# Kernel optimization log

Hardware: AMD Instinct MI355X
Metric: run time of the kernel (lower is better)

## Reference

```python
import jax, jax.numpy as jnp
import numpy as np

BS, SEQ, D_MODEL = 4, 1024, 4096
N_Q_HEADS, N_KV_HEADS, D_K, D_V = 32, 8, 128, 128
ROPE_BASE = 10000.0


def _rotate_half(x):
    x1, x2 = jnp.split(x, 2, axis=-1)
    return jnp.concatenate([-x2, x1], axis=-1)


def _apply_rope(x, pos0):
    # x: [bs, heads, seq, d]; positions pos0 .. pos0+seq-1
    d = x.shape[-1]
    seq = x.shape[2]
    inv_freq = 1.0 / (ROPE_BASE ** (jnp.arange(0, d, 2, dtype=jnp.float32) / d))  # [d/2]
    pos = (pos0 + jnp.arange(seq)).astype(jnp.float32)  # [seq]
    ang = pos[:, None] * inv_freq[None, :]  # [seq, d/2]
    cos = jnp.concatenate([jnp.cos(ang), jnp.cos(ang)], axis=-1)  # [seq, d]
    sin = jnp.concatenate([jnp.sin(ang), jnp.sin(ang)], axis=-1)
    return x * cos[None, None] + _rotate_half(x) * sin[None, None]


def setup_inputs() -> dict:
    key = jax.random.key(0)
    ks = jax.random.split(key, 8)
    w_scale = 0.02  # keep logits in a sane range (original uses raw normal init)
    return {
        "query": jax.random.normal(ks[0], (BS, SEQ, D_MODEL), dtype=jnp.float32),
        "key": jax.random.normal(ks[1], (BS, SEQ, D_MODEL), dtype=jnp.float32),
        "value": jax.random.normal(ks[2], (BS, SEQ, D_MODEL), dtype=jnp.float32),
        "mask": jnp.zeros((BS, SEQ, SEQ), dtype=jnp.float32),
        "wq": jax.random.normal(ks[3], (D_MODEL, N_Q_HEADS * D_K), dtype=jnp.float32) * w_scale,
        "wk": jax.random.normal(ks[4], (D_MODEL, N_KV_HEADS * D_K), dtype=jnp.float32) * w_scale,
        "wv": jax.random.normal(ks[5], (D_MODEL, N_KV_HEADS * D_V), dtype=jnp.float32) * w_scale,
        "wo": jax.random.normal(ks[6], (N_Q_HEADS * D_V, D_MODEL), dtype=jnp.float32) * w_scale,
        "curr_seq_pos": 0,
    }


def reference(query, key, value, mask, wq, wk, wv, wo, curr_seq_pos):
    bs, sq, _ = query.shape
    n_groups = N_Q_HEADS // N_KV_HEADS
    # projections -> [bs, heads, seq, d]
    q = (query @ wq).reshape(bs, sq, N_Q_HEADS, D_K).transpose((0, 2, 1, 3))
    sk = key.shape[1]
    k = (key @ wk).reshape(bs, sk, N_KV_HEADS, 1, D_K)
    k = jnp.repeat(k, n_groups, axis=3).reshape(bs, sk, N_Q_HEADS, D_K).transpose((0, 2, 1, 3))
    v = (value @ wv).reshape(bs, sk, N_KV_HEADS, 1, D_V)
    v = jnp.repeat(v, n_groups, axis=3).reshape(bs, sk, N_Q_HEADS, D_V).transpose((0, 2, 1, 3))
    scale = jnp.sqrt(jnp.float32(D_K))
    q = _apply_rope(q, curr_seq_pos)
    k = _apply_rope(k, curr_seq_pos)
    # [bs, h, sq, sk]
    raw = jnp.einsum("bhqd,bhkd->bhqk", q, k) / scale
    masked = raw + mask[:bs, None, curr_seq_pos:curr_seq_pos + sq, :sk]
    attn = jax.nn.softmax(masked, axis=-1)
    out = jnp.einsum("bhqk,bhkd->bhqd", attn, v)
    out = out.transpose((0, 2, 1, 3)).reshape(bs, sq, N_Q_HEADS * D_V)
    return out @ wo
```

## Files before the change

### kernel.cpp

```cpp
#include <hip/hip_runtime.h>


using ushort = unsigned short;
typedef __attribute__((ext_vector_type(8))) short short8;
typedef __attribute__((ext_vector_type(4))) short short4v;
typedef __attribute__((ext_vector_type(4))) float f32x4;

__device__ __forceinline__ ushort f2bf(float x) {
  unsigned int u = __float_as_uint(x);
  u += 0x7FFFu + ((u >> 16) & 1u);
  return (ushort)(u >> 16);
}
__device__ __forceinline__ float bf2f(ushort h) {
  return __uint_as_float(((unsigned int)h) << 16);
}

__device__ __forceinline__ void async_copy16(const void* g, void* l) {
  __builtin_amdgcn_global_load_lds((const __attribute__((address_space(1))) void*)g,
                                   (__attribute__((address_space(3))) void*)l, 16, 0, 0);
}

__global__ __launch_bounds__(256)
void cvt_f32_bf16(const float* __restrict__ in, ushort* __restrict__ out, int n4) {
  const int i = blockIdx.x * 256 + threadIdx.x;
  if (i < n4) {
    const float4 f = ((const float4*)in)[i];
    short4v v;
    v[0] = (short)f2bf(f.x); v[1] = (short)f2bf(f.y);
    v[2] = (short)f2bf(f.z); v[3] = (short)f2bf(f.w);
    ((short4v*)out)[i] = v;
  }
}

__global__ __launch_bounds__(256)
void transpose_cvt(const float* __restrict__ B, ushort* __restrict__ Bt, int N) {
  __shared__ ushort t[64][72];
  const int n0 = blockIdx.x * 64, k0 = blockIdx.y * 64;
  const int tid = threadIdx.x;
  const int r = tid >> 3, c8 = (tid & 7) * 8;
#pragma unroll
  for (int p = 0; p < 2; p++) {
    const float* src = B + (size_t)(k0 + r + p * 32) * N + n0 + c8;
    const float4 f0 = *(const float4*)src;
    const float4 f1 = *(const float4*)(src + 4);
    ushort* d = &t[r + p * 32][c8];
    d[0] = f2bf(f0.x); d[1] = f2bf(f0.y); d[2] = f2bf(f0.z); d[3] = f2bf(f0.w);
    d[4] = f2bf(f1.x); d[5] = f2bf(f1.y); d[6] = f2bf(f1.z); d[7] = f2bf(f1.w);
  }
  __syncthreads();
#pragma unroll
  for (int p = 0; p < 2; p++) {
    const int n = r + p * 32;
    short8 o;
#pragma unroll
    for (int j = 0; j < 8; j++) o[j] = (short)t[c8 + j][n];
    *(short8*)(Bt + (size_t)(n0 + n) * 4096 + k0 + c8) = o;
  }
}

template <int MODE, bool AF32>
__global__ __launch_bounds__(256, 2)
void gemm_bt(const float* __restrict__ Af, const float* __restrict__ A2f,
             const ushort* __restrict__ Abf, const ushort* __restrict__ Bt,
             ushort* __restrict__ C, ushort* __restrict__ C2,
             float* __restrict__ Cf, const int* __restrict__ posp,
             int N, float scale) {
  constexpr int K = 4096;
  __shared__ alignas(16) ushort As[128 * 32];
  __shared__ alignas(16) ushort Bs[128 * 32];
  const int tid = threadIdx.x;
  const int wave = tid >> 6, lane = tid & 63;
  const int quad = lane >> 4, l16 = lane & 15;
  const int m0 = blockIdx.y * 128, n0 = blockIdx.x * 128;
  const int wm = (wave & 1) * 64, wn2 = (wave >> 1) * 32;

  const size_t aoff = (size_t)(m0 + wave * 16 + (lane >> 2)) * K + (lane & 3) * 8;
  const float* gAf = nullptr;
  const ushort* gAb = nullptr;
  if constexpr (AF32) {
    const float* Ause = Af;
    if constexpr (MODE == 4) {
      if (n0 >= 1024) Ause = A2f;
    }
    gAf = Ause + aoff;
  } else {
    gAb = Abf + aoff;
  }
  const ushort* gB = Bt + (size_t)(n0 + wave * 16 + (lane >> 2)) * K + (lane & 3) * 8;
  ushort* lA = As + wave * 512;
  ushort* lB = Bs + wave * 512;
  constexpr size_t rstep = (size_t)64 * K;

  f32x4 acc[4][4] = {};

  for (int kt = 0; kt < K; kt += 32) {
    if constexpr (AF32) {
      const float4 a0 = *(const float4*)(gAf + kt);
      const float4 a1 = *(const float4*)(gAf + kt + 4);
      const float4 b0 = *(const float4*)(gAf + rstep + kt);
      const float4 b1 = *(const float4*)(gAf + rstep + kt + 4);
      short8 v0, v1;
      v0[0] = (short)f2bf(a0.x); v0[1] = (short)f2bf(a0.y);
      v0[2] = (short)f2bf(a0.z); v0[3] = (short)f2bf(a0.w);
      v0[4] = (short)f2bf(a1.x); v0[5] = (short)f2bf(a1.y);
      v0[6] = (short)f2bf(a1.z); v0[7] = (short)f2bf(a1.w);
      v1[0] = (short)f2bf(b0.x); v1[1] = (short)f2bf(b0.y);
      v1[2] = (short)f2bf(b0.z); v1[3] = (short)f2bf(b0.w);
      v1[4] = (short)f2bf(b1.x); v1[5] = (short)f2bf(b1.y);
      v1[6] = (short)f2bf(b1.z); v1[7] = (short)f2bf(b1.w);
      *(short8*)(lA + lane * 8) = v0;
      *(short8*)(lA + 2048 + lane * 8) = v1;
    } else {
      async_copy16(gAb + kt, lA);
      async_copy16(gAb + rstep + kt, lA + 2048);
    }
    async_copy16(gB + kt, lB);
    async_copy16(gB + rstep + kt, lB + 2048);
    __syncthreads();
    short8 af[4], bfrag[4];
#pragma unroll
    for (int i = 0; i < 4; i++) {
      af[i] = *(const short8*)(As + (wm + i * 16 + l16) * 32 + quad * 8);
      bfrag[i] = *(const short8*)(
          Bs + (wn2 + (i & 1) * 16 + (i >> 1) * 64 + l16) * 32 + quad * 8);
    }
#pragma unroll
    for (int i = 0; i < 4; i++)
#pragma unroll
      for (int j = 0; j < 4; j++)
        acc[i][j] = __builtin_amdgcn_mfma_f32_16x16x32_bf16(af[i], bfrag[j],
                                                            acc[i][j], 0, 0, 0);
    __syncthreads();
  }

  if constexpr (MODE == 0) {
#pragma unroll
    for (int i = 0; i < 4; i++)
#pragma unroll
      for (int j = 0; j < 4; j++) {
        const int n = n0 + wn2 + (j & 1) * 16 + (j >> 1) * 64 + l16;
        const int mb = m0 + wm + i * 16 + quad * 4;
#pragma unroll
        for (int r = 0; r < 4; r++)
          Cf[(size_t)(mb + r) * N + n] = acc[i][j][r] * scale;
      }
  } else {
    const bool kv_v = (MODE == 4) && (n0 >= 1024);
    if (!kv_v) {
      const int pos0 = posp[0];
      const int h = (MODE == 1) ? (n0 >> 7) : (n0 >> 7);
      const int NH = (MODE == 1) ? 32 : 8;
      constexpr float lgbase = -0.20762050593045983f;
      float invf[2];
      invf[0] = exp2f((float)(wn2 + l16) * lgbase);
      invf[1] = exp2f((float)(wn2 + 16 + l16) * lgbase);
#pragma unroll
      for (int i = 0; i < 4; i++) {
#pragma unroll
        for (int r = 0; r < 4; r++) {
          const int m = m0 + wm + i * 16 + quad * 4 + r;
          const int s = m & 1023, bb = m >> 10;
          const float p = (float)(s + pos0);
          ushort* row = C + (((size_t)bb * NH + h) * 1024 + s) * 128;
#pragma unroll
          for (int jj = 0; jj < 2; jj++) {
            float sn, cs;
            sincosf(p * invf[jj], &sn, &cs);
            const float x1 = acc[i][jj][r] * scale;
            const float x2 = acc[i][jj + 2][r] * scale;
            const int dlo = wn2 + jj * 16 + l16;
            row[dlo] = f2bf(x1 * cs - x2 * sn);
            row[dlo + 64] = f2bf(x2 * cs + x1 * sn);
          }
        }
      }
    } else {
      const int hh = (n0 - 1024) >> 7;
#pragma unroll
      for (int i = 0; i < 4; i++)
#pragma unroll
        for (int j = 0; j < 4; j++) {
          const int d = wn2 + (j & 1) * 16 + (j >> 1) * 64 + l16;
          const int mb = m0 + wm + i * 16 + quad * 4;
#pragma unroll
          for (int r = 0; r < 4; r++) {
            const int m = mb + r;
            const int bb = m >> 10, s = m & 1023;
            C2[(((size_t)bb * 8 + hh) * 128 + d) * 1024 + s] = f2bf(acc[i][j][r]);
          }
        }
    }
  }
}

__global__ __launch_bounds__(256, 2)
void attn_kernel(const ushort* __restrict__ Qh, const ushort* __restrict__ Kh,
                 const ushort* __restrict__ Vt, const ushort* __restrict__ Mk,
                 ushort* __restrict__ Oh) {
  __shared__ alignas(16) ushort Qs[64 * 128];
  __shared__ alignas(16) ushort Ks[64 * 128];
  __shared__ alignas(16) ushort Vs[128 * 64];
  __shared__ alignas(16) ushort Ms[64 * 64];
  ushort* Ps = Ks;
  const int b = blockIdx.z, h = blockIdx.y;
  const int q0 = blockIdx.x * 64;
  const int hkv = h >> 2;
  const int tid = threadIdx.x;
  const int wave = tid >> 6, lane = tid & 63;
  const int quad = lane >> 4, l16 = lane & 15;

  const ushort* Qg = Qh + (((size_t)b * 32 + h) * 1024 + q0) * 128;
  const ushort* Kg = Kh + ((size_t)b * 8 + hkv) * (size_t)(1024 * 128);
  const ushort* Vg = Vt + ((size_t)b * 8 + hkv) * (size_t)(128 * 1024);
  const ushort* Mg = Mk + ((size_t)b * 1024 + q0) * 1024;

#pragma unroll
  for (int c = 0; c < 4; c++) {
    const int i = wave * 4 + c;
    const int row = i * 4 + (lane >> 4);
    const int kc = (lane & 15) ^ (c * 4 + (lane >> 4));
    async_copy16(Qg + (size_t)row * 128 + kc * 8, Qs + i * 512);
  }

  float m_i[4], l_i[4];
#pragma unroll
  for (int r = 0; r < 4; r++) { m_i[r] = -1e30f; l_i[r] = 0.0f; }
  f32x4 acc_o[8] = {};

  const int vr = lane >> 3;
  const int vkc = (lane & 7) ^ (vr & 7);

  for (int kt = 0; kt < 1024; kt += 64) {
#pragma unroll
    for (int c = 0; c < 4; c++) {
      const int i = wave * 4 + c;
      const int row = i * 4 + (lane >> 4);
      const int kc = (lane & 15) ^ (c * 4 + (lane >> 4));
      async_copy16(Kg + (size_t)(kt + row) * 128 + kc * 8, Ks + i * 512);
    }
#pragma unroll
    for (int c = 0; c < 4; c++) {
      const int i = wave * 4 + c;
      async_copy16(Vg + (size_t)(i * 8 + vr) * 1024 + kt + vkc * 8, Vs + i * 512);
    }
#pragma unroll
    for (int c = 0; c < 2; c++)
      async_copy16(Mg + (size_t)(wave * 8 + c * 32 + vr) * 1024 + kt + (lane & 7) * 8,
                   Ms + wave * 512 + c * 2048);
    __syncthreads();

    f32x4 s[4] = {};
    const int qrow = (wave * 16 + l16) * 128;
#pragma unroll
    for (int ks = 0; ks < 4; ks++) {
      const int ko = ((ks * 4 + quad) ^ l16) * 8;
      const short8 aq = *(const short8*)(Qs + qrow + ko);
#pragma unroll
      for (int nt = 0; nt < 4; nt++) {
        const short8 bk = *(const short8*)(Ks + (nt * 16 + l16) * 128 + ko);
        s[nt] = __builtin_amdgcn_mfma_f32_16x16x32_bf16(aq, bk, s[nt], 0, 0, 0);
      }
    }
    __syncthreads();

#pragma unroll
    for (int nt = 0; nt < 4; nt++)
#pragma unroll
      for (int r = 0; r < 4; r++)
        s[nt][r] += bf2f(Ms[(wave * 16 + quad * 4 + r) * 64 + nt * 16 + l16]);

    float al[4];
#pragma unroll
    for (int r = 0; r < 4; r++) {
      float mx = fmaxf(fmaxf(s[0][r], s[1][r]), fmaxf(s[2][r], s[3][r]));
#pragma unroll
      for (int off = 1; off < 16; off <<= 1) mx = fmaxf(mx, __shfl_xor(mx, off));
      const float mnew = fmaxf(m_i[r], mx);
      al[r] = __expf(m_i[r] - mnew);
      float sum = 0.0f;
#pragma unroll
      for (int nt = 0; nt < 4; nt++) {
        const float pv = __expf(s[nt][r] - mnew);
        s[nt][r] = pv;
        sum += pv;
      }
#pragma unroll
      for (int off = 1; off < 16; off <<= 1) sum += __shfl_xor(sum, off);
      l_i[r] = l_i[r] * al[r] + sum;
      m_i[r] = mnew;
    }
#pragma unroll
    for (int dt = 0; dt < 8; dt++)
#pragma unroll
      for (int r = 0; r < 4; r++) acc_o[dt][r] *= al[r];

#pragma unroll
    for (int nt = 0; nt < 4; nt++)
#pragma unroll
      for (int r = 0; r < 4; r++)
        Ps[wave * 1152 + (quad * 4 + r) * 72 + nt * 16 + l16] = f2bf(s[nt][r]);
    __asm__ volatile("s_waitcnt lgkmcnt(0)" ::: "memory");

#pragma unroll
    for (int kk = 0; kk < 2; kk++) {
      const short8 ap = *(const short8*)(Ps + wave * 1152 + l16 * 72 + kk * 32 + quad * 8);
#pragma unroll
      for (int dt = 0; dt < 8; dt++) {
        const int vo = ((kk * 4 + quad) ^ (l16 & 7)) * 8;
        const short8 bv = *(const short8*)(Vs + (dt * 16 + l16) * 64 + vo);
        acc_o[dt] = __builtin_amdgcn_mfma_f32_16x16x32_bf16(ap, bv, acc_o[dt], 0, 0, 0);
      }
    }
    __syncthreads();
  }

  ushort* Og = Oh + ((size_t)b * 1024 + q0 + wave * 16) * 4096 + h * 128;
#pragma unroll
  for (int r = 0; r < 4; r++) {
    const float inv = 1.0f / l_i[r];
#pragma unroll
    for (int dt = 0; dt < 8; dt++)
      Og[(size_t)(quad * 4 + r) * 4096 + dt * 16 + l16] = f2bf(acc_o[dt][r] * inv);
  }
}

extern "C" void kernel_launch(void* const* d_in, const int* in_sizes, int n_in,
                              void* d_out, int out_size, void* d_ws, size_t ws_size,
                              hipStream_t stream) {
  (void)in_sizes; (void)n_in; (void)out_size; (void)ws_size;
  const float* query = (const float*)d_in[0];
  const float* key = (const float*)d_in[1];
  const float* value = (const float*)d_in[2];
  const float* mask = (const float*)d_in[3];
  const float* wq = (const float*)d_in[4];
  const float* wk = (const float*)d_in[5];
  const float* wv = (const float*)d_in[6];
  const float* wo = (const float*)d_in[7];
  const int* pos = (const int*)d_in[8];
  float* out = (float*)d_out;

  char* ws = (char*)d_ws;
  const size_t MB = 1024 * 1024;
  ushort* qb = (ushort*)(ws + 0 * MB);
  ushort* Khb = (ushort*)(ws + 0 * MB);
  ushort* Vtb = (ushort*)(ws + 8 * MB);
  ushort* wqT = (ushort*)(ws + 32 * MB);
  ushort* wkvT = (ushort*)(ws + 32 * MB);
  ushort* Ohb = (ushort*)(ws + 32 * MB);
  ushort* Qhb = (ushort*)(ws + 64 * MB);
  ushort* woT = (ushort*)(ws + 64 * MB);
  ushort* mbf = (ushort*)(ws + 96 * MB);

  dim3 blk(256);
  cvt_f32_bf16<<<dim3(4096), blk, 0, stream>>>(mask, mbf, 1048576);
  cvt_f32_bf16<<<dim3(16384), blk, 0, stream>>>(query, qb, 4194304);

  transpose_cvt<<<dim3(64, 64), blk, 0, stream>>>(wq, wqT, 4096);
  gemm_bt<1, false><<<dim3(32, 32), blk, 0, stream>>>(
      nullptr, nullptr, qb, wqT, Qhb, nullptr, nullptr, pos, 4096,
      0.08838834764831845f);

  transpose_cvt<<<dim3(16, 64), blk, 0, stream>>>(wk, wkvT, 1024);
  transpose_cvt<<<dim3(16, 64), blk, 0, stream>>>(wv, wkvT + (size_t)1024 * 4096, 1024);
  gemm_bt<4, true><<<dim3(16, 32), blk, 0, stream>>>(
      key, value, nullptr, wkvT, Khb, Vtb, nullptr, pos, 2048, 1.0f);

  attn_kernel<<<dim3(16, 32, 4), blk, 0, stream>>>(Qhb, Khb, Vtb, mbf, Ohb);

  transpose_cvt<<<dim3(64, 64), blk, 0, stream>>>(wo, woT, 4096);
  gemm_bt<0, false><<<dim3(32, 32), blk, 0, stream>>>(
      nullptr, nullptr, Ohb, woT, nullptr, nullptr, out, pos, 4096, 1.0f);
}
```

Measured before the change: 964.8 us.

## Restructure attention kernel with 128-row tiles, double-buffered K/V and lazy rescale

The attention kernel now processes 128 query rows per block (32 per wave) with Q held in registers. It double-buffers K/V tiles in LDS so the next tile loads while the current one computes, and reads the mask directly from global memory into registers. It skips the online-softmax rescale unless the row max grows by more than a threshold, defers the row-sum reduction to the end, and swizzles the P buffer. These changes cut per-iteration syncs and load latency and raise MFMA reuse of K/V, at the cost of more registers and possibly lower occupancy.

```diff
diff --git a/kernel.cpp b/kernel.cpp
--- a/kernel.cpp
+++ b/kernel.cpp
@@ -197,17 +197,22 @@
 void attn_kernel(const ushort* __restrict__ Qh, const ushort* __restrict__ Kh,
                  const ushort* __restrict__ Vt, const ushort* __restrict__ Mk,
                  ushort* __restrict__ Oh) {
-  __shared__ alignas(16) ushort Qs[64 * 128];
-  __shared__ alignas(16) ushort Ks[64 * 128];
-  __shared__ alignas(16) ushort Vs[128 * 64];
-  __shared__ alignas(16) ushort Ms[64 * 64];
-  ushort* Ps = Ks;
+  __shared__ alignas(16) ushort smem[40960];
+  ushort* const Ks0 = smem;
+  ushort* const Ks1 = smem + 8192;
+  ushort* const Vs0 = smem + 16384;
+  ushort* const Vs1 = smem + 24576;
+  ushort* const Ps = smem + 32768;
+  ushort* const Qtmp = smem + 16384;
+
   const int b = blockIdx.z, h = blockIdx.y;
-  const int q0 = blockIdx.x * 64;
+  const int q0 = blockIdx.x * 128;
   const int hkv = h >> 2;
   const int tid = threadIdx.x;
   const int wave = tid >> 6, lane = tid & 63;
   const int quad = lane >> 4, l16 = lane & 15;
+  const int vr = lane >> 3;
+  const int vkc = (lane & 7) ^ (vr & 7);
 
   const ushort* Qg = Qh + (((size_t)b * 32 + h) * 1024 + q0) * 128;
   const ushort* Kg = Kh + ((size_t)b * 8 + hkv) * (size_t)(1024 * 128);
@@ -215,113 +220,174 @@
   const ushort* Mg = Mk + ((size_t)b * 1024 + q0) * 1024;
 
 #pragma unroll
+  for (int c = 0; c < 8; c++) {
+    const int i = wave * 8 + c;
+    const int row = i * 4 + quad;
+    const int kc = l16 ^ ((c & 3) * 4 + quad);
+    async_copy16(Qg + (size_t)row * 128 + kc * 8, Qtmp + i * 512);
+  }
+#pragma unroll
   for (int c = 0; c < 4; c++) {
     const int i = wave * 4 + c;
-    const int row = i * 4 + (lane >> 4);
-    const int kc = (lane & 15) ^ (c * 4 + (lane >> 4));
-    async_copy16(Qg + (size_t)row * 128 + kc * 8, Qs + i * 512);
-  }
-
-  float m_i[4], l_i[4];
-#pragma unroll
-  for (int r = 0; r < 4; r++) { m_i[r] = -1e30f; l_i[r] = 0.0f; }
-  f32x4 acc_o[8] = {};
-
-  const int vr = lane >> 3;
-  const int vkc = (lane & 7) ^ (vr & 7);
+    const int row = i * 4 + quad;
+    const int kc = l16 ^ (c * 4 + quad);
+    async_copy16(Kg + (size_t)row * 128 + kc * 8, Ks0 + i * 512);
+  }
+  __asm__ volatile("s_waitcnt vmcnt(0)" ::: "memory");
+  short8 qreg[2][4];
+#pragma unroll
+  for (int t = 0; t < 2; t++)
+#pragma unroll
+    for (int ks = 0; ks < 4; ks++)
+      qreg[t][ks] = *(const short8*)(Qtmp + (size_t)(wave * 32 + t * 16 + l16) * 128 +
+                                     (((ks * 4 + quad) ^ l16) * 8));
+  __syncthreads();
+#pragma unroll
+  for (int c = 0; c < 4; c++) {
+    const int i = wave * 4 + c;
+    async_copy16(Vg + (size_t)(i * 8 + vr) * 1024 + vkc * 8, Vs0 + i * 512);
+  }
+
+  float m_i[2][4], l_p[2][4];
+#pragma unroll
+  for (int t = 0; t < 2; t++)
+#pragma unroll
+    for (int r = 0; r < 4; r++) { m_i[t][r] = -1e30f; l_p[t][r] = 0.0f; }
+  f32x4 acc[2][8] = {};
+
+  ushort* const PW = Ps + wave * 2048;
 
   for (int kt = 0; kt < 1024; kt += 64) {
-#pragma unroll
-    for (int c = 0; c < 4; c++) {
-      const int i = wave * 4 + c;
-      const int row = i * 4 + (lane >> 4);
-      const int kc = (lane & 15) ^ (c * 4 + (lane >> 4));
-      async_copy16(Kg + (size_t)(kt + row) * 128 + kc * 8, Ks + i * 512);
-    }
-#pragma unroll
-    for (int c = 0; c < 4; c++) {
-      const int i = wave * 4 + c;
-      async_copy16(Vg + (size_t)(i * 8 + vr) * 1024 + kt + vkc * 8, Vs + i * 512);
-    }
-#pragma unroll
-    for (int c = 0; c < 2; c++)
-      async_copy16(Mg + (size_t)(wave * 8 + c * 32 + vr) * 1024 + kt + (lane & 7) * 8,
-                   Ms + wave * 512 + c * 2048);
+    const int it = kt >> 6;
+    ushort* const Kc = (it & 1) ? Ks1 : Ks0;
+    ushort* const Vc = (it & 1) ? Vs1 : Vs0;
+    ushort* const Kn = (it & 1) ? Ks0 : Ks1;
+    ushort* const Vn = (it & 1) ? Vs0 : Vs1;
     __syncthreads();
 
-    f32x4 s[4] = {};
-    const int qrow = (wave * 16 + l16) * 128;
+    ushort mr[2][4][4];
+#pragma unroll
+    for (int t = 0; t < 2; t++)
+#pragma unroll
+      for (int nt = 0; nt < 4; nt++)
+#pragma unroll
+        for (int r = 0; r < 4; r++)
+          mr[t][nt][r] = Mg[(size_t)(wave * 32 + t * 16 + quad * 4 + r) * 1024 +
+                            kt + nt * 16 + l16];
+
+    f32x4 s0[4] = {}, s1[4] = {};
+    __builtin_amdgcn_s_setprio(1);
 #pragma unroll
     for (int ks = 0; ks < 4; ks++) {
       const int ko = ((ks * 4 + quad) ^ l16) * 8;
-      const short8 aq = *(const short8*)(Qs + qrow + ko);
 #pragma unroll
       for (int nt = 0; nt < 4; nt++) {
-        const short8 bk = *(const short8*)(Ks + (nt * 16 + l16) * 128 + ko);
-        s[nt] = __builtin_amdgcn_mfma_f32_16x16x32_bf16(aq, bk, s[nt], 0, 0, 0);
-      }
-    }
-    __syncthreads();
+        const short8 bk = *(const short8*)(Kc + (size_t)(nt * 16 + l16) * 128 + ko);
+        s0[nt] = __builtin_amdgcn_mfma_f32_16x16x32_bf16(qreg[0][ks], bk, s0[nt], 0, 0, 0);
+        s1[nt] = __builtin_amdgcn_mfma_f32_16x16x32_bf16(qreg[1][ks], bk, s1[nt], 0, 0, 0);
+      }
+    }
+    __builtin_amdgcn_s_setprio(0);
+
+    if (kt < 960) {
+#pragma unroll
+      for (int c = 0; c < 4; c++) {
+        const int i = wave * 4 + c;
+        const int row = i * 4 + quad;
+        const int kc = l16 ^ (c * 4 + quad);
+        async_copy16(Kg + (size_t)(kt + 64 + row) * 128 + kc * 8, Kn + i * 512);
+      }
+#pragma unroll
+      for (int c = 0; c < 4; c++) {
+        const int i = wave * 4 + c;
+        async_copy16(Vg + (size_t)(i * 8 + vr) * 1024 + kt + 64 + vkc * 8, Vn + i * 512);
+      }
+    }
 
 #pragma unroll
     for (int nt = 0; nt < 4; nt++)
 #pragma unroll
-      for (int r = 0; r < 4; r++)
-        s[nt][r] += bf2f(Ms[(wave * 16 + quad * 4 + r) * 64 + nt * 16 + l16]);
-
-    float al[4];
-#pragma unroll
-    for (int r = 0; r < 4; r++) {
-      float mx = fmaxf(fmaxf(s[0][r], s[1][r]), fmaxf(s[2][r], s[3][r]));
-#pragma unroll
-      for (int off = 1; off < 16; off <<= 1) mx = fmaxf(mx, __shfl_xor(mx, off));
-      const float mnew = fmaxf(m_i[r], mx);
-      al[r] = __expf(m_i[r] - mnew);
-      float sum = 0.0f;
-#pragma unroll
-      for (int nt = 0; nt < 4; nt++) {
-        const float pv = __expf(s[nt][r] - mnew);
-        s[nt][r] = pv;
-        sum += pv;
-      }
-#pragma unroll
-      for (int off = 1; off < 16; off <<= 1) sum += __shfl_xor(sum, off);
-      l_i[r] = l_i[r] * al[r] + sum;
-      m_i[r] = mnew;
-    }
-#pragma unroll
-    for (int dt = 0; dt < 8; dt++)
-#pragma unroll
-      for (int r = 0; r < 4; r++) acc_o[dt][r] *= al[r];
-
-#pragma unroll
-    for (int nt = 0; nt < 4; nt++)
-#pragma unroll
-      for (int r = 0; r < 4; r++)
-        Ps[wave * 1152 + (quad * 4 + r) * 72 + nt * 16 + l16] = f2bf(s[nt][r]);
+      for (int r = 0; r < 4; r++) {
+        s0[nt][r] += bf2f(mr[0][nt][r]);
+        s1[nt][r] += bf2f(mr[1][nt][r]);
+      }
+
+    float mx[2][4];
+    int need = 0;
+#pragma unroll
+    for (int t = 0; t < 2; t++)
+#pragma unroll
+      for (int r = 0; r < 4; r++) {
+        float v = t ? fmaxf(fmaxf(s1[0][r], s1[1][r]), fmaxf(s1[2][r], s1[3][r]))
+                    : fmaxf(fmaxf(s0[0][r], s0[1][r]), fmaxf(s0[2][r], s0[3][r]));
+#pragma unroll
+        for (int off = 1; off < 16; off <<= 1) v = fmaxf(v, __shfl_xor(v, off));
+        mx[t][r] = v;
+        need |= (v > m_i[t][r] + 8.0f) ? 1 : 0;
+      }
+    if (__any(need)) {
+#pragma unroll
+      for (int t = 0; t < 2; t++)
+#pragma unroll
+        for (int r = 0; r < 4; r++) {
+          const float mnew = fmaxf(m_i[t][r], mx[t][r]);
+          const float al = __expf(m_i[t][r] - mnew);
+          m_i[t][r] = mnew;
+          l_p[t][r] *= al;
+#pragma unroll
+          for (int dt = 0; dt < 8; dt++) acc[t][dt][r] *= al;
+        }
+    }
+
+#pragma unroll
+    for (int t = 0; t < 2; t++)
+#pragma unroll
+      for (int r = 0; r < 4; r++) {
+        const int prow = t * 16 + quad * 4 + r;
+        const int key8 = ((prow >> 1) & 7) * 8;
+        float sum = 0.0f;
+#pragma unroll
+        for (int nt = 0; nt < 4; nt++) {
+          const float sv = t ? s1[nt][r] : s0[nt][r];
+          const float p = __expf(sv - m_i[t][r]);
+          sum += p;
+          PW[prow * 64 + ((nt * 16 + l16) ^ key8)] = f2bf(p);
+        }
+        l_p[t][r] += sum;
+      }
     __asm__ volatile("s_waitcnt lgkmcnt(0)" ::: "memory");
 
+    __builtin_amdgcn_s_setprio(1);
 #pragma unroll
     for (int kk = 0; kk < 2; kk++) {
-      const short8 ap = *(const short8*)(Ps + wave * 1152 + l16 * 72 + kk * 32 + quad * 8);
+      const int pslot = ((kk * 4 + quad) ^ (l16 >> 1)) * 8;
+      const short8 ap0 = *(const short8*)(PW + (size_t)l16 * 64 + pslot);
+      const short8 ap1 = *(const short8*)(PW + (size_t)(16 + l16) * 64 + pslot);
 #pragma unroll
       for (int dt = 0; dt < 8; dt++) {
         const int vo = ((kk * 4 + quad) ^ (l16 & 7)) * 8;
-        const short8 bv = *(const short8*)(Vs + (dt * 16 + l16) * 64 + vo);
-        acc_o[dt] = __builtin_amdgcn_mfma_f32_16x16x32_bf16(ap, bv, acc_o[dt], 0, 0, 0);
-      }
-    }
-    __syncthreads();
-  }
-
-  ushort* Og = Oh + ((size_t)b * 1024 + q0 + wave * 16) * 4096 + h * 128;
-#pragma unroll
-  for (int r = 0; r < 4; r++) {
-    const float inv = 1.0f / l_i[r];
-#pragma unroll
-    for (int dt = 0; dt < 8; dt++)
-      Og[(size_t)(quad * 4 + r) * 4096 + dt * 16 + l16] = f2bf(acc_o[dt][r] * inv);
-  }
+        const short8 bv = *(const short8*)(Vc + (size_t)(dt * 16 + l16) * 64 + vo);
+        acc[0][dt] = __builtin_amdgcn_mfma_f32_16x16x32_bf16(ap0, bv, acc[0][dt], 0, 0, 0);
+        acc[1][dt] = __builtin_amdgcn_mfma_f32_16x16x32_bf16(ap1, bv, acc[1][dt], 0, 0, 0);
+      }
+    }
+    __builtin_amdgcn_s_setprio(0);
+  }
+
+  ushort* Og = Oh + ((size_t)b * 1024 + q0 + wave * 32) * 4096 + h * 128;
+#pragma unroll
+  for (int t = 0; t < 2; t++)
+#pragma unroll
+    for (int r = 0; r < 4; r++) {
+      float l = l_p[t][r];
+#pragma unroll
+      for (int off = 1; off < 16; off <<= 1) l += __shfl_xor(l, off);
+      const float inv = 1.0f / l;
+#pragma unroll
+      for (int dt = 0; dt < 8; dt++)
+        Og[(size_t)(t * 16 + quad * 4 + r) * 4096 + dt * 16 + l16] =
+            f2bf(acc[t][dt][r] * inv);
+    }
 }
 
 extern "C" void kernel_launch(void* const* d_in, const int* in_sizes, int n_in,
@@ -365,7 +431,7 @@
   gemm_bt<4, true><<<dim3(16, 32), blk, 0, stream>>>(
       key, value, nullptr, wkvT, Khb, Vtb, nullptr, pos, 2048, 1.0f);
 
-  attn_kernel<<<dim3(16, 32, 4), blk, 0, stream>>>(Qhb, Khb, Vtb, mbf, Ohb);
+  attn_kernel<<<dim3(8, 32, 4), blk, 0, stream>>>(Qhb, Khb, Vtb, mbf, Ohb);
 
   transpose_cvt<<<dim3(64, 64), blk, 0, stream>>>(wo, woT, 4096);
   gemm_bt<0, false><<<dim3(32, 32), blk, 0, stream>>>(
```

Measured after the change: 1.192 ms. 23.6% more time.
